# Optimization experiments

Measured on AMD Instinct MI355X. Metric: run time of the kernel, lower is better.

## Reference

```python
import jax, jax.numpy as jnp
import numpy as np

B, N, D = 4096, 64, 256  # batch, n_nodes, d_input


def setup_inputs() -> dict:
    key = jax.random.key(0)
    k = jax.random.split(key, 6)
    return {
        "x": jax.random.normal(k[0], (B, N, D), dtype=jnp.float32),
        "W1": jax.random.normal(k[1], (1,), dtype=jnp.float32),
        "W2": jax.random.normal(k[2], (D, 1), dtype=jnp.float32),
        "W3": jax.random.normal(k[3], (D,), dtype=jnp.float32),
        "bs": jax.random.normal(k[4], (1, N, N), dtype=jnp.float32),
        "Vs": jax.random.normal(k[5], (N, N), dtype=jnp.float32),
    }


def reference(x, W1, W2, W3, bs, Vs):
    # x: (B, N, D). Dropout is identity (inference / p=0).
    # LHS = (x * W1) @ W2  -> (B, N, 1); collapse to (B, N)
    lhs = jnp.einsum("bnd,d->bn", x, W2[:, 0]) * W1[0]
    # RHS = W3 @ x (over feature dim) -> (B, N); used as (B, 1, N)
    rhs = jnp.einsum("bnd,d->bn", x, W3)
    # scores: Vs @ tanh(outer(lhs, rhs) + bs)  -> (B, N, N)
    t = jnp.tanh(lhs[:, :, None] * rhs[:, None, :] + bs)  # (B, N, N)
    s = jnp.einsum("ij,bjk->bik", Vs, t)  # (B, N, N)
    # softmax over the flattened N*N scores per batch element
    a = jax.nn.softmax(s.reshape(x.shape[0], -1), axis=-1)
    return a.reshape(-1, N, N)
```

## Files before the change

### kernel.cpp

```cpp
#include <hip/hip_runtime.h>


typedef float f32x4 __attribute__((ext_vector_type(4)));
typedef __bf16 bf16x8 __attribute__((ext_vector_type(8)));

__global__ __launch_bounds__(256, 4) void adjatt_kernel(
    const float* __restrict__ x,
    const float* __restrict__ W1,
    const float* __restrict__ W2,
    const float* __restrict__ W3,
    const float* __restrict__ bs,
    const float* __restrict__ Vs,
    float* __restrict__ out)
{
    __shared__ __align__(16) unsigned char tT[16384];
    __shared__ __align__(16) float lhs[64];
    __shared__ __align__(16) float rhs[64];
    __shared__ float redm[4], reds[4];

    const int tid  = threadIdx.x;
    const int b    = blockIdx.x;
    const int lane = tid & 63;
    const int w    = tid >> 6;

    const float W1v = W1[0];

    bf16x8 Ah[2], Al[2];
    {
        const int row = 16 * w + (lane & 15);
        #pragma unroll
        for (int s = 0; s < 2; ++s) {
            const float* vp = Vs + row * 64 + 32 * s + 8 * (lane >> 4);
            f32x4 f0 = *(const f32x4*)vp;
            f32x4 f1 = *(const f32x4*)(vp + 4);
            #pragma unroll
            for (int e = 0; e < 4; ++e) {
                __bf16 h0 = (__bf16)f0[e];
                Ah[s][e] = h0;
                Al[s][e] = (__bf16)(f0[e] - (float)h0);
                __bf16 h1 = (__bf16)f1[e];
                Ah[s][e + 4] = h1;
                Al[s][e + 4] = (__bf16)(f1[e] - (float)h1);
            }
        }
    }

    {
        const int co = tid & 15;
        const int r0 = tid >> 4;
        f32x4 w2v[4], w3v[4];
        #pragma unroll
        for (int kk = 0; kk < 4; ++kk) {
            w2v[kk] = *(const f32x4*)(W2 + 4 * (co + 16 * kk));
            w3v[kk] = *(const f32x4*)(W3 + 4 * (co + 16 * kk));
        }
        const float* xb = x + (size_t)b * 16384;
        #pragma unroll
        for (int it = 0; it < 4; ++it) {
            const int r = r0 + 16 * it;
            const float* xr = xb + r * 256;
            float d2 = 0.f, d3 = 0.f;
            #pragma unroll
            for (int kk = 0; kk < 4; ++kk) {
                f32x4 xv = *(const f32x4*)(xr + 4 * (co + 16 * kk));
                d2 = fmaf(xv[0], w2v[kk][0], d2); d2 = fmaf(xv[1], w2v[kk][1], d2);
                d2 = fmaf(xv[2], w2v[kk][2], d2); d2 = fmaf(xv[3], w2v[kk][3], d2);
                d3 = fmaf(xv[0], w3v[kk][0], d3); d3 = fmaf(xv[1], w3v[kk][1], d3);
                d3 = fmaf(xv[2], w3v[kk][2], d3); d3 = fmaf(xv[3], w3v[kk][3], d3);
            }
            d2 += __shfl_xor(d2, 1); d2 += __shfl_xor(d2, 2);
            d2 += __shfl_xor(d2, 4); d2 += __shfl_xor(d2, 8);
            d3 += __shfl_xor(d3, 1); d3 += __shfl_xor(d3, 2);
            d3 += __shfl_xor(d3, 4); d3 += __shfl_xor(d3, 8);
            if (co == 0) { lhs[r] = d2 * W1v; rhs[r] = d3; }
        }
    }
    __syncthreads();

    {
        const int n  = lane;
        const int j0 = 16 * w;
        const float rv = rhs[n];
        f32x4 lh[4];
        #pragma unroll
        for (int c = 0; c < 4; ++c) lh[c] = *(const f32x4*)&lhs[j0 + 4 * c];
        bf16x8 hi[2], lo[2];
        #pragma unroll
        for (int jj = 0; jj < 16; ++jj) {
            float z  = fmaf(lh[jj >> 2][jj & 3], rv, bs[(j0 + jj) * 64 + n]);
            float e2 = __expf(2.f * z);
            float th = 1.f - __fdividef(2.f, e2 + 1.f);
            __bf16 h = (__bf16)th;
            hi[jj >> 3][jj & 7] = h;
            lo[jj >> 3][jj & 7] = (__bf16)(th - (float)h);
        }
        #pragma unroll
        for (int c = 0; c < 2; ++c) {
            const int off = (n * 128 + (j0 + 8 * c) * 2) ^ ((n & 7) << 4);
            *(bf16x8*)(tT + off)        = hi[c];
            *(bf16x8*)(tT + 8192 + off) = lo[c];
        }
    }
    __syncthreads();

    f32x4 acc[4];
    #pragma unroll
    for (int nt = 0; nt < 4; ++nt) acc[nt] = (f32x4){0.f, 0.f, 0.f, 0.f};
    #pragma unroll
    for (int nt = 0; nt < 4; ++nt) {
        const int n = 16 * nt + (lane & 15);
        #pragma unroll
        for (int s = 0; s < 2; ++s) {
            const int off = (n * 128 + 64 * s + 16 * (lane >> 4)) ^ ((n & 7) << 4);
            bf16x8 Bh = *(const bf16x8*)(tT + off);
            bf16x8 Bl = *(const bf16x8*)(tT + 8192 + off);
            acc[nt] = __builtin_amdgcn_mfma_f32_16x16x32_bf16(Ah[s], Bh, acc[nt], 0, 0, 0);
            acc[nt] = __builtin_amdgcn_mfma_f32_16x16x32_bf16(Al[s], Bh, acc[nt], 0, 0, 0);
            acc[nt] = __builtin_amdgcn_mfma_f32_16x16x32_bf16(Ah[s], Bl, acc[nt], 0, 0, 0);
        }
    }

    float m = acc[0][0];
    #pragma unroll
    for (int nt = 0; nt < 4; ++nt)
        #pragma unroll
        for (int e = 0; e < 4; ++e) m = fmaxf(m, acc[nt][e]);
    #pragma unroll
    for (int off = 1; off < 64; off <<= 1) m = fmaxf(m, __shfl_xor(m, off));
    if (lane == 0) redm[w] = m;
    __syncthreads();
    const float M = fmaxf(fmaxf(redm[0], redm[1]), fmaxf(redm[2], redm[3]));

    float ssum = 0.f;
    #pragma unroll
    for (int nt = 0; nt < 4; ++nt)
        #pragma unroll
        for (int e = 0; e < 4; ++e) {
            acc[nt][e] = __expf(acc[nt][e] - M);
            ssum += acc[nt][e];
        }
    #pragma unroll
    for (int off = 1; off < 64; off <<= 1) ssum += __shfl_xor(ssum, off);
    if (lane == 0) reds[w] = ssum;
    __syncthreads();
    const float inv = __fdividef(1.f, reds[0] + reds[1] + reds[2] + reds[3]);

    float* ob = out + (size_t)b * 4096;
    const int rbase = 16 * w + 4 * (lane >> 4);
    const int cbase = lane & 15;
    #pragma unroll
    for (int nt = 0; nt < 4; ++nt) {
        const int col = 16 * nt + cbase;
        #pragma unroll
        for (int e = 0; e < 4; ++e) {
            ob[(rbase + e) * 64 + col] = acc[nt][e] * inv;
        }
    }
}

extern "C" void kernel_launch(void* const* d_in, const int* in_sizes, int n_in,
                              void* d_out, int out_size, void* d_ws, size_t ws_size,
                              hipStream_t stream) {
    const float* x  = (const float*)d_in[0];
    const float* W1 = (const float*)d_in[1];
    const float* W2 = (const float*)d_in[2];
    const float* W3 = (const float*)d_in[3];
    const float* bs = (const float*)d_in[4];
    const float* Vs = (const float*)d_in[5];
    float* out = (float*)d_out;

    const int B = in_sizes[0] / (64 * 256);
    adjatt_kernel<<<dim3(B), dim3(256), 0, stream>>>(x, W1, W2, W3, bs, Vs, out);
}
```

Baseline: 69.74 us.

## Split dot-product stage into separate kernel staging lhs/rhs through output buffer

Moves the per-row x·W2 and x·W3 reductions into a standalone kernel that gives each group of four lanes a whole row, and writes lhs/rhs into the first 128 floats of each batch's output slice. The attention kernel then reads those values back instead of streaming x itself, which keeps its register and occupancy profile focused on the tanh/MFMA/softmax work. The dots kernel is meant to run as a purely bandwidth-bound pass over x with higher occupancy. In exchange it adds a second launch and an extra global round trip through the output buffer.

```diff
diff --git a/kernel.cpp b/kernel.cpp
--- a/kernel.cpp
+++ b/kernel.cpp
@@ -4,11 +4,48 @@
 typedef float f32x4 __attribute__((ext_vector_type(4)));
 typedef __bf16 bf16x8 __attribute__((ext_vector_type(8)));
 
-__global__ __launch_bounds__(256, 4) void adjatt_kernel(
+__global__ __launch_bounds__(256, 8) void adjatt_dots(
     const float* __restrict__ x,
     const float* __restrict__ W1,
     const float* __restrict__ W2,
     const float* __restrict__ W3,
+    float* __restrict__ out,
+    int R)
+{
+    const int lane = threadIdx.x & 63;
+    const int w    = threadIdx.x >> 6;
+    const int gw   = blockIdx.x * 4 + w;
+    const int q    = lane & 3;
+    const int rsub = lane >> 2;
+    const float W1v = W1[0];
+
+    #pragma unroll
+    for (int g = 0; g < 2; ++g) {
+        const int r = gw * 32 + g * 16 + rsub;
+        if (r >= R) break;
+        const float* xr = x + (size_t)r * 256 + q * 4;
+        float d2 = 0.f, d3 = 0.f;
+        #pragma unroll
+        for (int c = 0; c < 16; ++c) {
+            f32x4 xv = *(const f32x4*)(xr + c * 16);
+            f32x4 w2 = *(const f32x4*)(W2 + c * 16 + q * 4);
+            f32x4 w3 = *(const f32x4*)(W3 + c * 16 + q * 4);
+            d2 = fmaf(xv[0], w2[0], d2); d2 = fmaf(xv[1], w2[1], d2);
+            d2 = fmaf(xv[2], w2[2], d2); d2 = fmaf(xv[3], w2[3], d2);
+            d3 = fmaf(xv[0], w3[0], d3); d3 = fmaf(xv[1], w3[1], d3);
+            d3 = fmaf(xv[2], w3[2], d3); d3 = fmaf(xv[3], w3[3], d3);
+        }
+        d2 += __shfl_xor(d2, 1); d2 += __shfl_xor(d2, 2);
+        d3 += __shfl_xor(d3, 1); d3 += __shfl_xor(d3, 2);
+        if (q == 0) {
+            const int b = r >> 6, n = r & 63;
+            out[(size_t)b * 4096 + n]      = d2 * W1v;
+            out[(size_t)b * 4096 + 64 + n] = d3;
+        }
+    }
+}
+
+__global__ __launch_bounds__(256, 4) void adjatt_attn(
     const float* __restrict__ bs,
     const float* __restrict__ Vs,
     float* __restrict__ out)
@@ -23,7 +60,10 @@
     const int lane = tid & 63;
     const int w    = tid >> 6;
 
-    const float W1v = W1[0];
+    if (tid < 128) {
+        float v = out[(size_t)b * 4096 + tid];
+        if (tid < 64) lhs[tid] = v; else rhs[tid - 64] = v;
+    }
 
     bf16x8 Ah[2], Al[2];
     {
@@ -42,37 +82,6 @@
                 Ah[s][e + 4] = h1;
                 Al[s][e + 4] = (__bf16)(f1[e] - (float)h1);
             }
-        }
-    }
-
-    {
-        const int co = tid & 15;
-        const int r0 = tid >> 4;
-        f32x4 w2v[4], w3v[4];
-        #pragma unroll
-        for (int kk = 0; kk < 4; ++kk) {
-            w2v[kk] = *(const f32x4*)(W2 + 4 * (co + 16 * kk));
-            w3v[kk] = *(const f32x4*)(W3 + 4 * (co + 16 * kk));
-        }
-        const float* xb = x + (size_t)b * 16384;
-        #pragma unroll
-        for (int it = 0; it < 4; ++it) {
-            const int r = r0 + 16 * it;
-            const float* xr = xb + r * 256;
-            float d2 = 0.f, d3 = 0.f;
-            #pragma unroll
-            for (int kk = 0; kk < 4; ++kk) {
-                f32x4 xv = *(const f32x4*)(xr + 4 * (co + 16 * kk));
-                d2 = fmaf(xv[0], w2v[kk][0], d2); d2 = fmaf(xv[1], w2v[kk][1], d2);
-                d2 = fmaf(xv[2], w2v[kk][2], d2); d2 = fmaf(xv[3], w2v[kk][3], d2);
-                d3 = fmaf(xv[0], w3v[kk][0], d3); d3 = fmaf(xv[1], w3v[kk][1], d3);
-                d3 = fmaf(xv[2], w3v[kk][2], d3); d3 = fmaf(xv[3], w3v[kk][3], d3);
-            }
-            d2 += __shfl_xor(d2, 1); d2 += __shfl_xor(d2, 2);
-            d2 += __shfl_xor(d2, 4); d2 += __shfl_xor(d2, 8);
-            d3 += __shfl_xor(d3, 1); d3 += __shfl_xor(d3, 2);
-            d3 += __shfl_xor(d3, 4); d3 += __shfl_xor(d3, 8);
-            if (co == 0) { lhs[r] = d2 * W1v; rhs[r] = d3; }
         }
     }
     __syncthreads();
@@ -170,5 +179,9 @@
     float* out = (float*)d_out;
 
     const int B = in_sizes[0] / (64 * 256);
-    adjatt_kernel<<<dim3(B), dim3(256), 0, stream>>>(x, W1, W2, W3, bs, Vs, out);
+    const int R = B * 64;
+    const int grid1 = (R + 127) / 128;
+
+    adjatt_dots<<<dim3(grid1), dim3(256), 0, stream>>>(x, W1, W2, W3, out, R);
+    adjatt_attn<<<dim3(B), dim3(256), 0, stream>>>(bs, Vs, out);
 }
```

Result: slower. 91.15 us (+30.7%).

## Swap MFMA operand order for vectorized stores, restructure projection loads, raise occupancy

Applied to the files above, without the earlier changes.

The MFMA operands are swapped, with the tanh tile as A and Vs as B. Each lane now holds four consecutive output columns, so the final softmax write becomes 16-byte vector stores instead of scalar strided stores. The x projection is rewritten so each group of four threads reduces one row with 16 vector loads, which needs fewer shuffles. Launch bounds rise to 6 blocks per CU, which limits registers per thread to gain occupancy and could cause spills.

```diff
diff --git a/kernel.cpp b/kernel.cpp
--- a/kernel.cpp
+++ b/kernel.cpp
@@ -4,7 +4,7 @@
 typedef float f32x4 __attribute__((ext_vector_type(4)));
 typedef __bf16 bf16x8 __attribute__((ext_vector_type(8)));
 
-__global__ __launch_bounds__(256, 4) void adjatt_kernel(
+__global__ __launch_bounds__(256, 6) void adjatt_kernel(
     const float* __restrict__ x,
     const float* __restrict__ W1,
     const float* __restrict__ W2,
@@ -22,10 +22,32 @@
     const int b    = blockIdx.x;
     const int lane = tid & 63;
     const int w    = tid >> 6;
-
     const float W1v = W1[0];
 
-    bf16x8 Ah[2], Al[2];
+    {
+        const int r = tid >> 2;
+        const int q = tid & 3;
+        const float* xr  = x + (size_t)b * 16384 + r * 256 + q * 4;
+        const float* w2p = W2 + q * 4;
+        const float* w3p = W3 + q * 4;
+        float d2 = 0.f, d3 = 0.f;
+        #pragma unroll 4
+        for (int c = 0; c < 16; ++c) {
+            f32x4 xv = *(const f32x4*)(xr + c * 16);
+            f32x4 w2 = *(const f32x4*)(w2p + c * 16);
+            f32x4 w3 = *(const f32x4*)(w3p + c * 16);
+            d2 = fmaf(xv[0], w2[0], d2); d2 = fmaf(xv[1], w2[1], d2);
+            d2 = fmaf(xv[2], w2[2], d2); d2 = fmaf(xv[3], w2[3], d2);
+            d3 = fmaf(xv[0], w3[0], d3); d3 = fmaf(xv[1], w3[1], d3);
+            d3 = fmaf(xv[2], w3[2], d3); d3 = fmaf(xv[3], w3[3], d3);
+        }
+        d2 += __shfl_xor(d2, 1); d2 += __shfl_xor(d2, 2);
+        d3 += __shfl_xor(d3, 1); d3 += __shfl_xor(d3, 2);
+        if (q == 0) { lhs[r] = d2 * W1v; rhs[r] = d3; }
+    }
+    __syncthreads();
+
+    bf16x8 Vh[2], Vl[2];
     {
         const int row = 16 * w + (lane & 15);
         #pragma unroll
@@ -36,46 +58,14 @@
             #pragma unroll
             for (int e = 0; e < 4; ++e) {
                 __bf16 h0 = (__bf16)f0[e];
-                Ah[s][e] = h0;
-                Al[s][e] = (__bf16)(f0[e] - (float)h0);
+                Vh[s][e] = h0;
+                Vl[s][e] = (__bf16)(f0[e] - (float)h0);
                 __bf16 h1 = (__bf16)f1[e];
-                Ah[s][e + 4] = h1;
-                Al[s][e + 4] = (__bf16)(f1[e] - (float)h1);
+                Vh[s][e + 4] = h1;
+                Vl[s][e + 4] = (__bf16)(f1[e] - (float)h1);
             }
         }
     }
-
-    {
-        const int co = tid & 15;
-        const int r0 = tid >> 4;
-        f32x4 w2v[4], w3v[4];
-        #pragma unroll
-        for (int kk = 0; kk < 4; ++kk) {
-            w2v[kk] = *(const f32x4*)(W2 + 4 * (co + 16 * kk));
-            w3v[kk] = *(const f32x4*)(W3 + 4 * (co + 16 * kk));
-        }
-        const float* xb = x + (size_t)b * 16384;
-        #pragma unroll
-        for (int it = 0; it < 4; ++it) {
-            const int r = r0 + 16 * it;
-            const float* xr = xb + r * 256;
-            float d2 = 0.f, d3 = 0.f;
-            #pragma unroll
-            for (int kk = 0; kk < 4; ++kk) {
-                f32x4 xv = *(const f32x4*)(xr + 4 * (co + 16 * kk));
-                d2 = fmaf(xv[0], w2v[kk][0], d2); d2 = fmaf(xv[1], w2v[kk][1], d2);
-                d2 = fmaf(xv[2], w2v[kk][2], d2); d2 = fmaf(xv[3], w2v[kk][3], d2);
-                d3 = fmaf(xv[0], w3v[kk][0], d3); d3 = fmaf(xv[1], w3v[kk][1], d3);
-                d3 = fmaf(xv[2], w3v[kk][2], d3); d3 = fmaf(xv[3], w3v[kk][3], d3);
-            }
-            d2 += __shfl_xor(d2, 1); d2 += __shfl_xor(d2, 2);
-            d2 += __shfl_xor(d2, 4); d2 += __shfl_xor(d2, 8);
-            d3 += __shfl_xor(d3, 1); d3 += __shfl_xor(d3, 2);
-            d3 += __shfl_xor(d3, 4); d3 += __shfl_xor(d3, 8);
-            if (co == 0) { lhs[r] = d2 * W1v; rhs[r] = d3; }
-        }
-    }
-    __syncthreads();
 
     {
         const int n  = lane;
@@ -105,26 +95,26 @@
 
     f32x4 acc[4];
     #pragma unroll
-    for (int nt = 0; nt < 4; ++nt) acc[nt] = (f32x4){0.f, 0.f, 0.f, 0.f};
+    for (int ct = 0; ct < 4; ++ct) acc[ct] = (f32x4){0.f, 0.f, 0.f, 0.f};
     #pragma unroll
-    for (int nt = 0; nt < 4; ++nt) {
-        const int n = 16 * nt + (lane & 15);
+    for (int ct = 0; ct < 4; ++ct) {
+        const int n = 16 * ct + (lane & 15);
         #pragma unroll
-        for (int s = 0; s < 2; ++s) {
-            const int off = (n * 128 + 64 * s + 16 * (lane >> 4)) ^ ((n & 7) << 4);
-            bf16x8 Bh = *(const bf16x8*)(tT + off);
-            bf16x8 Bl = *(const bf16x8*)(tT + 8192 + off);
-            acc[nt] = __builtin_amdgcn_mfma_f32_16x16x32_bf16(Ah[s], Bh, acc[nt], 0, 0, 0);
-            acc[nt] = __builtin_amdgcn_mfma_f32_16x16x32_bf16(Al[s], Bh, acc[nt], 0, 0, 0);
-            acc[nt] = __builtin_amdgcn_mfma_f32_16x16x32_bf16(Ah[s], Bl, acc[nt], 0, 0, 0);
+        for (int sk = 0; sk < 2; ++sk) {
+            const int off = (n * 128 + 64 * sk + 16 * (lane >> 4)) ^ ((n & 7) << 4);
+            bf16x8 Th = *(const bf16x8*)(tT + off);
+            bf16x8 Tl = *(const bf16x8*)(tT + 8192 + off);
+            acc[ct] = __builtin_amdgcn_mfma_f32_16x16x32_bf16(Th, Vh[sk], acc[ct], 0, 0, 0);
+            acc[ct] = __builtin_amdgcn_mfma_f32_16x16x32_bf16(Tl, Vh[sk], acc[ct], 0, 0, 0);
+            acc[ct] = __builtin_amdgcn_mfma_f32_16x16x32_bf16(Th, Vl[sk], acc[ct], 0, 0, 0);
         }
     }
 
     float m = acc[0][0];
     #pragma unroll
-    for (int nt = 0; nt < 4; ++nt)
+    for (int ct = 0; ct < 4; ++ct)
         #pragma unroll
-        for (int e = 0; e < 4; ++e) m = fmaxf(m, acc[nt][e]);
+        for (int e = 0; e < 4; ++e) m = fmaxf(m, acc[ct][e]);
     #pragma unroll
     for (int off = 1; off < 64; off <<= 1) m = fmaxf(m, __shfl_xor(m, off));
     if (lane == 0) redm[w] = m;
@@ -133,11 +123,11 @@
 
     float ssum = 0.f;
     #pragma unroll
-    for (int nt = 0; nt < 4; ++nt)
+    for (int ct = 0; ct < 4; ++ct)
         #pragma unroll
         for (int e = 0; e < 4; ++e) {
-            acc[nt][e] = __expf(acc[nt][e] - M);
-            ssum += acc[nt][e];
+            acc[ct][e] = __expf(acc[ct][e] - M);
+            ssum += acc[ct][e];
         }
     #pragma unroll
     for (int off = 1; off < 64; off <<= 1) ssum += __shfl_xor(ssum, off);
@@ -145,16 +135,11 @@
     __syncthreads();
     const float inv = __fdividef(1.f, reds[0] + reds[1] + reds[2] + reds[3]);
 
-    float* ob = out + (size_t)b * 4096;
-    const int rbase = 16 * w + 4 * (lane >> 4);
-    const int cbase = lane & 15;
+    float* ob = out + (size_t)b * 4096 + (16 * w + (lane & 15)) * 64 + 4 * (lane >> 4);
     #pragma unroll
-    for (int nt = 0; nt < 4; ++nt) {
-        const int col = 16 * nt + cbase;
-        #pragma unroll
-        for (int e = 0; e < 4; ++e) {
-            ob[(rbase + e) * 64 + col] = acc[nt][e] * inv;
-        }
+    for (int ct = 0; ct < 4; ++ct) {
+        f32x4 v = {acc[ct][0] * inv, acc[ct][1] * inv, acc[ct][2] * inv, acc[ct][3] * inv};
+        *(f32x4*)(ob + 16 * ct) = v;
     }
 }
 
```

Measured after the change: 74.54 us. 1.07x slower.

## Persistent 1024-thread kernel with double-buffered async x loads into LDS

Applied to the files above, without the earlier changes.

Turns the kernel into a persistent one: 256 blocks of 1024 threads loop over batch elements. Each step prefetches the next 64 KB x slice into LDS with global_load_lds while the current slice is computed. The tanh tile is now built in registers and fed straight to the MFMA as the A operand, with Vs as the B operand, so the LDS round-trip for the tanh matrix is gone. bs is cached once per block and stored with row padding. The cost is 128 KB+ of LDS per block, which allows one block per CU, plus manual waitcnt and barriers, and per-batch softmax reductions now span 16 waves.

```diff
diff --git a/kernel.cpp b/kernel.cpp
--- a/kernel.cpp
+++ b/kernel.cpp
@@ -4,65 +4,109 @@
 typedef float f32x4 __attribute__((ext_vector_type(4)));
 typedef __bf16 bf16x8 __attribute__((ext_vector_type(8)));
 
-__global__ __launch_bounds__(256, 4) void adjatt_kernel(
+typedef __attribute__((address_space(1))) const void gas1_void;
+typedef __attribute__((address_space(3))) void las3_void;
+
+#define GLOAD16(gp, lp) \
+    __builtin_amdgcn_global_load_lds((gas1_void*)(gp), (las3_void*)(lp), 16, 0, 0)
+
+#define WAIT_LGKM0_BAR()                                         \
+    do {                                                         \
+        asm volatile("s_waitcnt lgkmcnt(0)" ::: "memory");       \
+        __builtin_amdgcn_s_barrier();                            \
+        __builtin_amdgcn_sched_barrier(0);                       \
+    } while (0)
+
+__global__ __launch_bounds__(1024, 4) void adjatt_kernel(
     const float* __restrict__ x,
     const float* __restrict__ W1,
     const float* __restrict__ W2,
     const float* __restrict__ W3,
     const float* __restrict__ bs,
     const float* __restrict__ Vs,
-    float* __restrict__ out)
+    float* __restrict__ out,
+    int B)
 {
-    __shared__ __align__(16) unsigned char tT[16384];
-    __shared__ __align__(16) float lhs[64];
-    __shared__ __align__(16) float rhs[64];
-    __shared__ float redm[4], reds[4];
+    __shared__ __align__(16) float xbuf[2][16384];
+    __shared__ __align__(16) float xbs[64 * 65];
+    __shared__ __align__(16) float lr2[64][2];
+    __shared__ float redm[16], reds[16];
 
     const int tid  = threadIdx.x;
-    const int b    = blockIdx.x;
     const int lane = tid & 63;
     const int w    = tid >> 6;
+    const int l15  = lane & 15;
+    const int g    = lane >> 4;
+    const int rb   = w & 3;
+    const int cb   = w >> 2;
+    const int bid  = blockIdx.x;
 
+    f32x4 w2v[4], w3v[4];
+#pragma unroll
+    for (int kk = 0; kk < 4; ++kk) {
+        w2v[kk] = *(const f32x4*)(W2 + 4 * (l15 + 16 * kk));
+        w3v[kk] = *(const f32x4*)(W3 + 4 * (l15 + 16 * kk));
+    }
+    f32x4 vf0[2], vf1[2];
+#pragma unroll
+    for (int sk = 0; sk < 2; ++sk) {
+        const float* vp = Vs + (16 * rb + l15) * 64 + 32 * sk + 8 * g;
+        vf0[sk] = *(const f32x4*)vp;
+        vf1[sk] = *(const f32x4*)(vp + 4);
+    }
+    f32x4 bsv = *(const f32x4*)(bs + 4 * tid);
     const float W1v = W1[0];
 
-    bf16x8 Ah[2], Al[2];
-    {
-        const int row = 16 * w + (lane & 15);
-        #pragma unroll
-        for (int s = 0; s < 2; ++s) {
-            const float* vp = Vs + row * 64 + 32 * s + 8 * (lane >> 4);
-            f32x4 f0 = *(const f32x4*)vp;
-            f32x4 f1 = *(const f32x4*)(vp + 4);
-            #pragma unroll
-            for (int e = 0; e < 4; ++e) {
-                __bf16 h0 = (__bf16)f0[e];
-                Ah[s][e] = h0;
-                Al[s][e] = (__bf16)(f0[e] - (float)h0);
-                __bf16 h1 = (__bf16)f1[e];
-                Ah[s][e + 4] = h1;
-                Al[s][e + 4] = (__bf16)(f1[e] - (float)h1);
-            }
+    if (bid < B) {
+        const float* xs = x + (size_t)bid * 16384;
+#pragma unroll
+        for (int i = 0; i < 4; ++i)
+            GLOAD16(xs + (4 * w + i) * 256 + lane * 4, &xbuf[0][(4 * w + i) * 256]);
+    }
+
+    bf16x8 Vh[2], Vl[2];
+#pragma unroll
+    for (int sk = 0; sk < 2; ++sk) {
+#pragma unroll
+        for (int e = 0; e < 4; ++e) {
+            __bf16 h0 = (__bf16)vf0[sk][e];
+            Vh[sk][e] = h0;
+            Vl[sk][e] = (__bf16)(vf0[sk][e] - (float)h0);
+            __bf16 h1 = (__bf16)vf1[sk][e];
+            Vh[sk][e + 4] = h1;
+            Vl[sk][e + 4] = (__bf16)(vf1[sk][e] - (float)h1);
         }
     }
 
     {
-        const int co = tid & 15;
-        const int r0 = tid >> 4;
-        f32x4 w2v[4], w3v[4];
-        #pragma unroll
-        for (int kk = 0; kk < 4; ++kk) {
-            w2v[kk] = *(const f32x4*)(W2 + 4 * (co + 16 * kk));
-            w3v[kk] = *(const f32x4*)(W3 + 4 * (co + 16 * kk));
+        const int row = tid >> 4, col = 4 * (tid & 15);
+#pragma unroll
+        for (int e = 0; e < 4; ++e) xbs[row * 65 + col + e] = bsv[e];
+    }
+    WAIT_LGKM0_BAR();
+
+    int it = 0;
+    for (int b = bid; b < B; b += 256, ++it) {
+        const int cur = it & 1;
+        const int bn  = b + 256;
+
+        asm volatile("s_waitcnt vmcnt(0)" ::: "memory");
+        __builtin_amdgcn_sched_barrier(0);
+
+        if (bn < B) {
+            const float* xs = x + (size_t)bn * 16384;
+#pragma unroll
+            for (int i = 0; i < 4; ++i)
+                GLOAD16(xs + (4 * w + i) * 256 + lane * 4,
+                        &xbuf[cur ^ 1][(4 * w + i) * 256]);
         }
-        const float* xb = x + (size_t)b * 16384;
-        #pragma unroll
-        for (int it = 0; it < 4; ++it) {
-            const int r = r0 + 16 * it;
-            const float* xr = xb + r * 256;
+
+        {
             float d2 = 0.f, d3 = 0.f;
-            #pragma unroll
+            const float* xr = &xbuf[cur][(4 * w + g) * 256 + l15 * 4];
+#pragma unroll
             for (int kk = 0; kk < 4; ++kk) {
-                f32x4 xv = *(const f32x4*)(xr + 4 * (co + 16 * kk));
+                f32x4 xv = *(const f32x4*)(xr + kk * 64);
                 d2 = fmaf(xv[0], w2v[kk][0], d2); d2 = fmaf(xv[1], w2v[kk][1], d2);
                 d2 = fmaf(xv[2], w2v[kk][2], d2); d2 = fmaf(xv[3], w2v[kk][3], d2);
                 d3 = fmaf(xv[0], w3v[kk][0], d3); d3 = fmaf(xv[1], w3v[kk][1], d3);
@@ -72,89 +116,60 @@
             d2 += __shfl_xor(d2, 4); d2 += __shfl_xor(d2, 8);
             d3 += __shfl_xor(d3, 1); d3 += __shfl_xor(d3, 2);
             d3 += __shfl_xor(d3, 4); d3 += __shfl_xor(d3, 8);
-            if (co == 0) { lhs[r] = d2 * W1v; rhs[r] = d3; }
+            if (l15 == 0) {
+                lr2[4 * w + g][0] = d2 * W1v;
+                lr2[4 * w + g][1] = d3;
+            }
         }
-    }
-    __syncthreads();
+        WAIT_LGKM0_BAR();
 
-    {
-        const int n  = lane;
-        const int j0 = 16 * w;
-        const float rv = rhs[n];
-        f32x4 lh[4];
-        #pragma unroll
-        for (int c = 0; c < 4; ++c) lh[c] = *(const f32x4*)&lhs[j0 + 4 * c];
-        bf16x8 hi[2], lo[2];
-        #pragma unroll
-        for (int jj = 0; jj < 16; ++jj) {
-            float z  = fmaf(lh[jj >> 2][jj & 3], rv, bs[(j0 + jj) * 64 + n]);
-            float e2 = __expf(2.f * z);
-            float th = 1.f - __fdividef(2.f, e2 + 1.f);
-            __bf16 h = (__bf16)th;
-            hi[jj >> 3][jj & 7] = h;
-            lo[jj >> 3][jj & 7] = (__bf16)(th - (float)h);
+        const int n  = 16 * cb + l15;
+        const float rv = lr2[n][1];
+        f32x4 acc = (f32x4){0.f, 0.f, 0.f, 0.f};
+#pragma unroll
+        for (int sk = 0; sk < 2; ++sk) {
+            const int jb = 32 * sk + 8 * g;
+            bf16x8 Th, Tl;
+#pragma unroll
+            for (int e = 0; e < 8; ++e) {
+                float z  = fmaf(lr2[jb + e][0], rv, xbs[(jb + e) * 65 + n]);
+                float e2 = __expf(2.f * z);
+                float th = 1.f - __fdividef(2.f, e2 + 1.f);
+                __bf16 h = (__bf16)th;
+                Th[e] = h;
+                Tl[e] = (__bf16)(th - (float)h);
+            }
+            acc = __builtin_amdgcn_mfma_f32_16x16x32_bf16(Th, Vh[sk], acc, 0, 0, 0);
+            acc = __builtin_amdgcn_mfma_f32_16x16x32_bf16(Tl, Vh[sk], acc, 0, 0, 0);
+            acc = __builtin_amdgcn_mfma_f32_16x16x32_bf16(Th, Vl[sk], acc, 0, 0, 0);
         }
-        #pragma unroll
-        for (int c = 0; c < 2; ++c) {
-            const int off = (n * 128 + (j0 + 8 * c) * 2) ^ ((n & 7) << 4);
-            *(bf16x8*)(tT + off)        = hi[c];
-            *(bf16x8*)(tT + 8192 + off) = lo[c];
+
+        float m = fmaxf(fmaxf(acc[0], acc[1]), fmaxf(acc[2], acc[3]));
+#pragma unroll
+        for (int off = 1; off < 64; off <<= 1) m = fmaxf(m, __shfl_xor(m, off));
+        if (lane == 0) redm[w] = m;
+        WAIT_LGKM0_BAR();
+        float M = redm[l15];
+#pragma unroll
+        for (int off = 1; off < 16; off <<= 1) M = fmaxf(M, __shfl_xor(M, off));
+
+        float ssum = 0.f;
+#pragma unroll
+        for (int e = 0; e < 4; ++e) {
+            acc[e] = __expf(acc[e] - M);
+            ssum += acc[e];
         }
-    }
-    __syncthreads();
+#pragma unroll
+        for (int off = 1; off < 64; off <<= 1) ssum += __shfl_xor(ssum, off);
+        if (lane == 0) reds[w] = ssum;
+        WAIT_LGKM0_BAR();
+        float S = reds[l15];
+#pragma unroll
+        for (int off = 1; off < 16; off <<= 1) S += __shfl_xor(S, off);
+        const float inv = __fdividef(1.f, S);
 
-    f32x4 acc[4];
-    #pragma unroll
-    for (int nt = 0; nt < 4; ++nt) acc[nt] = (f32x4){0.f, 0.f, 0.f, 0.f};
-    #pragma unroll
-    for (int nt = 0; nt < 4; ++nt) {
-        const int n = 16 * nt + (lane & 15);
-        #pragma unroll
-        for (int s = 0; s < 2; ++s) {
-            const int off = (n * 128 + 64 * s + 16 * (lane >> 4)) ^ ((n & 7) << 4);
-            bf16x8 Bh = *(const bf16x8*)(tT + off);
-            bf16x8 Bl = *(const bf16x8*)(tT + 8192 + off);
-            acc[nt] = __builtin_amdgcn_mfma_f32_16x16x32_bf16(Ah[s], Bh, acc[nt], 0, 0, 0);
-            acc[nt] = __builtin_amdgcn_mfma_f32_16x16x32_bf16(Al[s], Bh, acc[nt], 0, 0, 0);
-            acc[nt] = __builtin_amdgcn_mfma_f32_16x16x32_bf16(Ah[s], Bl, acc[nt], 0, 0, 0);
-        }
-    }
-
-    float m = acc[0][0];
-    #pragma unroll
-    for (int nt = 0; nt < 4; ++nt)
-        #pragma unroll
-        for (int e = 0; e < 4; ++e) m = fmaxf(m, acc[nt][e]);
-    #pragma unroll
-    for (int off = 1; off < 64; off <<= 1) m = fmaxf(m, __shfl_xor(m, off));
-    if (lane == 0) redm[w] = m;
-    __syncthreads();
-    const float M = fmaxf(fmaxf(redm[0], redm[1]), fmaxf(redm[2], redm[3]));
-
-    float ssum = 0.f;
-    #pragma unroll
-    for (int nt = 0; nt < 4; ++nt)
-        #pragma unroll
-        for (int e = 0; e < 4; ++e) {
-            acc[nt][e] = __expf(acc[nt][e] - M);
-            ssum += acc[nt][e];
-        }
-    #pragma unroll
-    for (int off = 1; off < 64; off <<= 1) ssum += __shfl_xor(ssum, off);
-    if (lane == 0) reds[w] = ssum;
-    __syncthreads();
-    const float inv = __fdividef(1.f, reds[0] + reds[1] + reds[2] + reds[3]);
-
-    float* ob = out + (size_t)b * 4096;
-    const int rbase = 16 * w + 4 * (lane >> 4);
-    const int cbase = lane & 15;
-    #pragma unroll
-    for (int nt = 0; nt < 4; ++nt) {
-        const int col = 16 * nt + cbase;
-        #pragma unroll
-        for (int e = 0; e < 4; ++e) {
-            ob[(rbase + e) * 64 + col] = acc[nt][e] * inv;
-        }
+        f32x4 v = {acc[0] * inv, acc[1] * inv, acc[2] * inv, acc[3] * inv};
+        *(f32x4*)(out + (size_t)b * 4096 + (16 * rb + l15) * 64 + 16 * cb + 4 * g) = v;
     }
 }
 
@@ -170,5 +185,6 @@
     float* out = (float*)d_out;
 
     const int B = in_sizes[0] / (64 * 256);
-    adjatt_kernel<<<dim3(B), dim3(256), 0, stream>>>(x, W1, W2, W3, bs, Vs, out);
+    const int grid = (B < 256) ? B : 256;
+    adjatt_kernel<<<dim3(grid), dim3(1024), 0, stream>>>(x, W1, W2, W3, bs, Vs, out, B);
 }
```

After: 114.9 us. 64.7% more time.
